# Kernel tuning notes

Hardware: AMD Instinct MI355X
Metric: run time of the kernel (lower is better)

The kernel has to match this reference:

```python
import jax, jax.numpy as jnp
import numpy as np

V = 32000
MASK_ID = 31999
EPS = 1e-3          # log-linear schedule eps
DT = 0.05           # reverse-step size
NUCLEUS_P = 0.9
NEG_INF = -1000000.0
B, S = 2, 1024


def move_chance(t):
    # BD3-LM log-linear schedule: move_chance(t) = (1 - eps) * t
    return (1.0 - EPS) * t


def nucleus_filter(probs, p):
    # descending sort over vocab
    order = jnp.argsort(-probs, axis=-1)                     # [B,S,V]
    sorted_probs = jnp.take_along_axis(probs, order, axis=-1)
    cum = jnp.cumsum(sorted_probs, axis=-1)
    keep = cum <= p
    keep = keep.at[..., 0].set(True)                          # always keep top-1
    kept = sorted_probs * keep
    inv = jnp.argsort(order, axis=-1)                         # inverse permutation
    filtered = jnp.take_along_axis(kept, inv, axis=-1)        # scatter back
    return filtered / jnp.sum(filtered, axis=-1, keepdims=True)


def setup_inputs() -> dict:
    key = jax.random.key(0)
    k1, k2, k3, k4 = jax.random.split(key, 4)
    x = jax.random.randint(k1, (B, S), 0, V, dtype=jnp.int32)
    m = jax.random.uniform(k4, (B, S)) < 0.5
    x = jnp.where(m, MASK_ID, x)
    logits = jax.random.normal(k2, (B, S, V), dtype=jnp.float32)
    t = jnp.ones((1,), dtype=jnp.float32)
    u = jax.random.uniform(k3, (B, S, V), dtype=jnp.float32)
    return {"x": x, "logits": logits, "t": t, "u": u}


def reference(x, logits, t, u):
    mct = move_chance(t)[..., None]          # [1,1]
    mcs = move_chance(t - DT)[..., None]     # [1,1]
    mask_prob = mcs / mct                    # [1,1], broadcasts over [S,V]

    logits = logits.at[:, :, MASK_ID].set(NEG_INF)
    p_x0 = jax.nn.softmax(logits, axis=-1)   # [B,S,V]
    p_x0 = nucleus_filter(p_x0, NUCLEUS_P)

    q_xs = p_x0 * (1.0 - mask_prob)
    q_xs = q_xs.at[:, :, MASK_ID].set(jnp.squeeze(mask_prob, -1))

    gumbel = -jnp.log(-jnp.log(u + 1e-10) + 1e-10)
    x_new = jnp.argmax(q_xs / (gumbel + 1e-10), axis=-1).astype(x.dtype)

    is_masked = x == MASK_ID
    x_new = jnp.where(is_masked, x_new, x)
    return x_new, p_x0
```

## Files before the change

kernel.cpp:

```cpp
#include <hip/hip_runtime.h>

#define NVOC 32000
#define NV4  (NVOC / 4)
#define MASKID 31999
#define NBINS2 2048
#define NTHR 512
#define NWAVES (NTHR / 64)
#define LISTCAP 2048

typedef unsigned int u32;
typedef unsigned long long u64;

__device__ __forceinline__ u32 fix32(float e) {
    float x = e * 4294967296.0f;
    x = fminf(x, 4294967040.0f);
    return (u32)x;
}

__device__ __forceinline__ int zbin(float t) {
    int b = (int)floorf(t);
    b = b < 0 ? 0 : b;
    return b > (NBINS2 - 1) ? (NBINS2 - 1) : b;
}
__device__ __forceinline__ float elq(float t, int b) {
    return __expf((t - (float)(b + 1)) * 0.015625f);
}

__global__ __launch_bounds__(NTHR, 8) void mdlm_kernel(
    const int* __restrict__ xin,
    const float* __restrict__ logits,
    const float* __restrict__ tin,
    const float* __restrict__ uin,
    float* __restrict__ out,
    int rows)
{
    __shared__ u64 sHist[NBINS2];
    __shared__ float sTab[NBINS2];
    __shared__ u32 sList[LISTCAP];
    __shared__ double sRedD[NWAVES];
    __shared__ int sRedI[NWAVES];
    __shared__ float sTT;
    __shared__ int sCnt, sB, sCross, sMaxDrop, sBref;
    __shared__ u32 sTau;
    __shared__ u64 sPart;
    __shared__ double sAsD, sSfpD, sScaleB;

    double* sD = (double*)sHist;

    const int row = blockIdx.x;
    if (row >= rows) return;
    const int tid = threadIdx.x;
    const float4* lrow4 = (const float4*)(logits + (size_t)row * NVOC);
    const float4* urow4 = (const float4*)(uin + (size_t)row * NVOC);
    float* prow = out + (size_t)rows + (size_t)row * NVOC;

#pragma unroll
    for (int k = 0; k < 4; ++k) sHist[tid + k * NTHR] = 0ULL;
    if (tid == 0) {
        sCnt = 0; sB = -1; sCross = 0; sMaxDrop = -1; sBref = -1;
        sTau = 0xFFFFFFFFu; sPart = 0ULL;
        sTT = tin[0];
    }
    __syncthreads();

    for (int v4 = tid; v4 < NV4; v4 += NTHR) {
        float4 f = lrow4[v4];
        if (v4 == (MASKID >> 2)) f.w = -1000000.0f;
        float zz[4] = {f.x, f.y, f.z, f.w};
#pragma unroll
        for (int e4 = 0; e4 < 4; ++e4) {
            float t = fmaf(zz[e4], 64.0f, 1024.0f);
            int b = zbin(t);
            u32 m = fix32(elq(t, b));
            atomicAdd(&sHist[b], (u64)m);
        }
    }
    __syncthreads();

#pragma unroll
    for (int k = 0; k < 4; ++k) {
        int s = tid + k * NTHR;
        if (sHist[s] != 0ULL) atomicMax(&sBref, s);
    }
    __syncthreads();
    const int bref = sBref;

#pragma unroll
    for (int k = 0; k < 4; ++k) {
        int s = tid + k * NTHR;
        double sc = exp((double)(s - bref) * 0.015625);
        sTab[s] = (float)sc;
        u64 H = sHist[s];
        sD[s] = (double)H * sc;
    }
    __syncthreads();

    for (int dlt = 1; dlt < NBINS2; dlt <<= 1) {
        double a0 = (tid + dlt < NBINS2) ? sD[tid + dlt] : 0.0;
        double a1 = (tid + NTHR + dlt < NBINS2) ? sD[tid + NTHR + dlt] : 0.0;
        double a2 = (tid + 2 * NTHR + dlt < NBINS2) ? sD[tid + 2 * NTHR + dlt] : 0.0;
        double a3 = (tid + 3 * NTHR + dlt < NBINS2) ? sD[tid + 3 * NTHR + dlt] : 0.0;
        __syncthreads();
        sD[tid] += a0;
        sD[tid + NTHR] += a1;
        sD[tid + 2 * NTHR] += a2;
        sD[tid + 3 * NTHR] += a3;
        __syncthreads();
    }
    const double T = 0.9 * sD[0];

#pragma unroll
    for (int k = 0; k < 4; ++k) {
        int s = tid + k * NTHR;
        double Ai = sD[s];
        double As = (s + 1 < NBINS2) ? sD[s + 1] : 0.0;
        bool dropped = (As >= T);
        bool keptf = (Ai <= T);
        if (dropped) atomicMax(&sMaxDrop, s);
        if (!dropped && !keptf) { sB = s; sCross = 1; }
    }
    __syncthreads();
    if (tid == 0) {
        int B = sCross ? sB : sMaxDrop;
        sB = B;
        double As = (B + 1 < NBINS2) ? sD[B + 1] : 0.0;
        if (B < 0) As = sD[0];
        sAsD = As;
        sSfpD = As;
        sScaleB = (B >= 0) ? exp((double)(B - bref) * 0.015625) : 1.0;
    }
    __syncthreads();

    const int Bst = sB;
    const int cross = sCross;
    const double AsD = sAsD;
    const double dScaleB = sScaleB;

    if (cross) {
        for (int v4 = tid; v4 < NV4; v4 += NTHR) {
            float4 f = lrow4[v4];
            if (v4 == (MASKID >> 2)) f.w = -1000000.0f;
            float zz[4] = {f.x, f.y, f.z, f.w};
#pragma unroll
            for (int e4 = 0; e4 < 4; ++e4) {
                float t = fmaf(zz[e4], 64.0f, 1024.0f);
                int b = zbin(t);
                if (b == Bst) {
                    u32 m = fix32(elq(t, b));
                    int pos = atomicAdd(&sCnt, 1);
                    if (pos < LISTCAP) sList[pos] = m;
                }
            }
        }
        __syncthreads();
        const int K = sCnt < LISTCAP ? sCnt : LISTCAP;
        for (int jj = tid; jj < K; jj += NTHR) {
            u32 mj = sList[jj];
            u64 isum = 0ULL;
            for (int q2 = 0; q2 < K; ++q2) {
                u32 mv = sList[q2];
                if (mv >= mj) isum += (u64)mv;
            }
            double s = AsD + (double)isum * dScaleB;
            if (s <= T) atomicMin(&sTau, mj);
        }
        __syncthreads();
        u32 tl = sTau;
        if (tl != 0xFFFFFFFFu) {
            u64 part = 0ULL;
            for (int q2 = tid; q2 < K; q2 += NTHR) {
                u32 mv = sList[q2];
                if (mv >= tl) part += (u64)mv;
            }
            if (part) atomicAdd(&sPart, part);
        }
        __syncthreads();
        if (tid == 0 && tl != 0xFFFFFFFFu)
            sSfpD = AsD + (double)sPart * dScaleB;
        __syncthreads();
    }

    const u32 tauU = (cross && sTau != 0xFFFFFFFFu) ? sTau : 0xFFFFFFFFu;
    const double SfpD = sSfpD;
    const float invSf = (float)(4294967296.0 / SfpD);

#pragma unroll
    for (int k = 0; k < 4; ++k) {
        int s = tid + k * NTHR;
        sTab[s] *= invSf;
    }

    double mpd, omd;
    {
        double td = (double)sTT;
        mpd = ((1.0 - 1e-3) * (td - 0.05)) / ((1.0 - 1e-3) * td);
        omd = 1.0 - mpd;
    }
    const float mqf = (float)(mpd / omd);
    __syncthreads();

    float r1 = -3.0e38f, r2 = -3.0e38f;
    float q1 = 0.0f,     q2 = 0.0f;
    int   i1 = 0,        i2 = 0;
    for (int v4 = tid; v4 < NV4; v4 += NTHR) {
        float4 uf = urow4[v4];
        float4 f = lrow4[v4];
        if (v4 == (MASKID >> 2)) f.w = -1000000.0f;
        float zz[4] = {f.x, f.y, f.z, f.w};
        float uu[4] = {uf.x, uf.y, uf.z, uf.w};
        float pp[4];
        const int i0 = v4 * 4;
#pragma unroll
        for (int e4 = 0; e4 < 4; ++e4) {
            float t = fmaf(zz[e4], 64.0f, 1024.0f);
            int b = zbin(t);
            float el = elq(t, b);
            bool kept = (b > Bst) || (b == Bst && fix32(el) >= tauU);
            float p = kept ? el * sTab[b] : 0.0f;
            pp[e4] = p;
            float g = -__logf(1e-10f - __logf(uu[e4] + 1e-10f));
            float r = p * __builtin_amdgcn_rcpf(g + 1e-10f);
            if (r > r1)      { r2 = r1; q2 = q1; i2 = i1; r1 = r; q1 = p; i1 = i0 + e4; }
            else if (r > r2) { r2 = r;  q2 = p;  i2 = i0 + e4; }
        }
        float4 po;
        po.x = pp[0]; po.y = pp[1]; po.z = pp[2]; po.w = pp[3];
        ((float4*)prow)[v4] = po;
    }
    if (tid == ((MASKID >> 2) % NTHR)) {
        float um = ((const float*)urow4)[MASKID];
        float g = -__logf(1e-10f - __logf(um + 1e-10f));
        float rm = mqf * __builtin_amdgcn_rcpf(g + 1e-10f);
        if (rm > r1)      { r2 = r1; q2 = q1; i2 = i1; r1 = rm; q1 = 0.0f; i1 = MASKID; }
        else if (rm > r2) { r2 = rm; q2 = 0.0f; i2 = MASKID; }
    }

    double best; int bidx;
    {
        const float* urowf = (const float*)urow4;
        double qa = (i1 == MASKID) ? mpd : (double)q1 * omd;
        double g1 = -log(-log((double)urowf[i1] + 1e-10) + 1e-10);
        best = qa / (g1 + 1e-10);
        bidx = i1;
        double qb = (i2 == MASKID) ? mpd : (double)q2 * omd;
        double g2 = -log(-log((double)urowf[i2] + 1e-10) + 1e-10);
        double rd = qb / (g2 + 1e-10);
        if (rd > best || (rd == best && i2 < bidx)) { best = rd; bidx = i2; }
    }

    for (int off = 32; off > 0; off >>= 1) {
        double ov = __shfl_down(best, off, 64);
        int oi = __shfl_down(bidx, off, 64);
        if (ov > best || (ov == best && oi < bidx)) { best = ov; bidx = oi; }
    }
    if ((tid & 63) == 0) { sRedD[tid >> 6] = best; sRedI[tid >> 6] = bidx; }
    __syncthreads();
    if (tid == 0) {
        best = sRedD[0]; bidx = sRedI[0];
        for (int w = 1; w < NWAVES; ++w) {
            double ov = sRedD[w]; int oi = sRedI[w];
            if (ov > best || (ov == best && oi < bidx)) { best = ov; bidx = oi; }
        }
        int xv = xin[row];
        out[row] = (float)((xv == MASKID) ? bidx : xv);
    }
}

extern "C" void kernel_launch(void* const* d_in, const int* in_sizes, int n_in,
                              void* d_out, int out_size, void* d_ws, size_t ws_size,
                              hipStream_t stream) {
    const int* x = (const int*)d_in[0];
    const float* logits = (const float*)d_in[1];
    const float* t = (const float*)d_in[2];
    const float* u = (const float*)d_in[3];
    float* out = (float*)d_out;
    const int rows = in_sizes[0];
    hipLaunchKernelGGL(mdlm_kernel, dim3(rows), dim3(NTHR), 0, stream,
                       x, logits, t, u, out, rows);
}
```

Measured before the change: 257.8 us.

## Prune Gumbel argmax to candidates with u near 1/e, with exact fallback

The main vocab loop no longer computes the double-log Gumbel noise and a running top-2 for every element. It records the max kept probability and collects indices whose u lies in a narrow band around 1/e, where the Gumbel denominator is close to zero and the ratio is largest. The argmax is then evaluated exactly, in double precision, over that candidate list plus the mask token. If the winner does not clear a bound of qmax*(1-mask_prob)*100, or the list overflows, a full second pass re-reads u and the written probabilities to compute the exact argmax. This removes transcendental work from the hot loop, at the cost of shared-memory atomics, extra barriers and an occasional second full pass.

```diff
diff --git a/kernel.cpp b/kernel.cpp
--- a/kernel.cpp
+++ b/kernel.cpp
@@ -7,6 +7,10 @@
 #define NTHR 512
 #define NWAVES (NTHR / 64)
 #define LISTCAP 2048
+
+#define ULO_F 0.36419f
+#define UHI_F 0.37157f
+#define INV_G0 100.0
 
 typedef unsigned int u32;
 typedef unsigned long long u64;
@@ -39,8 +43,9 @@
     __shared__ u32 sList[LISTCAP];
     __shared__ double sRedD[NWAVES];
     __shared__ int sRedI[NWAVES];
-    __shared__ float sTT;
-    __shared__ int sCnt, sB, sCross, sMaxDrop, sBref;
+    __shared__ float sRedF[NWAVES];
+    __shared__ float sTT, sQmaxF;
+    __shared__ int sCnt, sCntB, sB, sCross, sMaxDrop, sBref, sNeed;
     __shared__ u32 sTau;
     __shared__ u64 sPart;
     __shared__ double sAsD, sSfpD, sScaleB;
@@ -52,13 +57,14 @@
     const int tid = threadIdx.x;
     const float4* lrow4 = (const float4*)(logits + (size_t)row * NVOC);
     const float4* urow4 = (const float4*)(uin + (size_t)row * NVOC);
+    const float* urowf = (const float*)urow4;
     float* prow = out + (size_t)rows + (size_t)row * NVOC;
 
 #pragma unroll
     for (int k = 0; k < 4; ++k) sHist[tid + k * NTHR] = 0ULL;
     if (tid == 0) {
-        sCnt = 0; sB = -1; sCross = 0; sMaxDrop = -1; sBref = -1;
-        sTau = 0xFFFFFFFFu; sPart = 0ULL;
+        sCnt = 0; sCntB = 0; sB = -1; sCross = 0; sMaxDrop = -1; sBref = -1;
+        sTau = 0xFFFFFFFFu; sPart = 0ULL; sNeed = 0;
         sTT = tin[0];
     }
     __syncthreads();
@@ -181,14 +187,10 @@
     }
 
     const u32 tauU = (cross && sTau != 0xFFFFFFFFu) ? sTau : 0xFFFFFFFFu;
-    const double SfpD = sSfpD;
-    const float invSf = (float)(4294967296.0 / SfpD);
-
-#pragma unroll
-    for (int k = 0; k < 4; ++k) {
-        int s = tid + k * NTHR;
-        sTab[s] *= invSf;
-    }
+    const float invSf = (float)(4294967296.0 / sSfpD);
+
+#pragma unroll
+    for (int k = 0; k < 4; ++k) sTab[tid + k * NTHR] *= invSf;
 
     double mpd, omd;
     {
@@ -196,12 +198,9 @@
         mpd = ((1.0 - 1e-3) * (td - 0.05)) / ((1.0 - 1e-3) * td);
         omd = 1.0 - mpd;
     }
-    const float mqf = (float)(mpd / omd);
-    __syncthreads();
-
-    float r1 = -3.0e38f, r2 = -3.0e38f;
-    float q1 = 0.0f,     q2 = 0.0f;
-    int   i1 = 0,        i2 = 0;
+    __syncthreads();
+
+    float maxp = 0.0f;
     for (int v4 = tid; v4 < NV4; v4 += NTHR) {
         float4 uf = urow4[v4];
         float4 f = lrow4[v4];
@@ -218,36 +217,47 @@
             bool kept = (b > Bst) || (b == Bst && fix32(el) >= tauU);
             float p = kept ? el * sTab[b] : 0.0f;
             pp[e4] = p;
-            float g = -__logf(1e-10f - __logf(uu[e4] + 1e-10f));
-            float r = p * __builtin_amdgcn_rcpf(g + 1e-10f);
-            if (r > r1)      { r2 = r1; q2 = q1; i2 = i1; r1 = r; q1 = p; i1 = i0 + e4; }
-            else if (r > r2) { r2 = r;  q2 = p;  i2 = i0 + e4; }
+            maxp = fmaxf(maxp, p);
+            if (uu[e4] >= ULO_F && uu[e4] <= UHI_F) {
+                int pos = atomicAdd(&sCntB, 1);
+                if (pos < LISTCAP) sList[pos] = (u32)(i0 + e4);
+            }
         }
         float4 po;
         po.x = pp[0]; po.y = pp[1]; po.z = pp[2]; po.w = pp[3];
         ((float4*)prow)[v4] = po;
     }
-    if (tid == ((MASKID >> 2) % NTHR)) {
-        float um = ((const float*)urow4)[MASKID];
-        float g = -__logf(1e-10f - __logf(um + 1e-10f));
-        float rm = mqf * __builtin_amdgcn_rcpf(g + 1e-10f);
-        if (rm > r1)      { r2 = r1; q2 = q1; i2 = i1; r1 = rm; q1 = 0.0f; i1 = MASKID; }
-        else if (rm > r2) { r2 = rm; q2 = 0.0f; i2 = MASKID; }
-    }
-
-    double best; int bidx;
+    __syncthreads();
+
+    for (int off = 32; off > 0; off >>= 1)
+        maxp = fmaxf(maxp, __shfl_down(maxp, off, 64));
+    if ((tid & 63) == 0) sRedF[tid >> 6] = maxp;
+    __syncthreads();
+    if (tid == 0) {
+        float m = sRedF[0];
+        for (int w = 1; w < NWAVES; ++w) m = fmaxf(m, sRedF[w]);
+        sQmaxF = m;
+    }
+
+    double best = -1.0e300; int bidx = NVOC;
     {
-        const float* urowf = (const float*)urow4;
-        double qa = (i1 == MASKID) ? mpd : (double)q1 * omd;
-        double g1 = -log(-log((double)urowf[i1] + 1e-10) + 1e-10);
-        best = qa / (g1 + 1e-10);
-        bidx = i1;
-        double qb = (i2 == MASKID) ? mpd : (double)q2 * omd;
-        double g2 = -log(-log((double)urowf[i2] + 1e-10) + 1e-10);
-        double rd = qb / (g2 + 1e-10);
-        if (rd > best || (rd == best && i2 < bidx)) { best = rd; bidx = i2; }
-    }
-
+        const int K = sCntB < LISTCAP ? sCntB : LISTCAP;
+        for (int jj = tid; jj < K; jj += NTHR) {
+            int i = (int)sList[jj];
+            float up = urowf[i];
+            float pf = prow[i];
+            double q = (double)pf * omd;
+            double g = -log(-log((double)up + 1e-10) + 1e-10);
+            double r = q / (g + 1e-10);
+            if (r > best || (r == best && i < bidx)) { best = r; bidx = i; }
+        }
+        if (tid == 0) {
+            float um = urowf[MASKID];
+            double gm = -log(-log((double)um + 1e-10) + 1e-10);
+            double rm = mpd / (gm + 1e-10);
+            if (rm > best || (rm == best && MASKID < bidx)) { best = rm; bidx = MASKID; }
+        }
+    }
     for (int off = 32; off > 0; off >>= 1) {
         double ov = __shfl_down(best, off, 64);
         int oi = __shfl_down(bidx, off, 64);
@@ -261,8 +271,49 @@
             double ov = sRedD[w]; int oi = sRedI[w];
             if (ov > best || (ov == best && oi < bidx)) { best = ov; bidx = oi; }
         }
-        int xv = xin[row];
-        out[row] = (float)((xv == MASKID) ? bidx : xv);
+        double bound = (double)sQmaxF * omd * INV_G0;
+        int need = (sCntB > LISTCAP) || !(best > bound);
+        sNeed = need;
+        if (!need) {
+            int xv = xin[row];
+            out[row] = (float)((xv == MASKID) ? bidx : xv);
+        }
+    }
+    __syncthreads();
+
+    if (sNeed) {
+        double fb = -1.0e300; int fi = NVOC;
+        for (int v4 = tid; v4 < NV4; v4 += NTHR) {
+            float4 uf = urow4[v4];
+            float4 pf4 = ((const float4*)prow)[v4];
+            float uu[4] = {uf.x, uf.y, uf.z, uf.w};
+            float pp[4] = {pf4.x, pf4.y, pf4.z, pf4.w};
+            const int i0 = v4 * 4;
+#pragma unroll
+            for (int e4 = 0; e4 < 4; ++e4) {
+                const int i = i0 + e4;
+                double q = (i == MASKID) ? mpd : (double)pp[e4] * omd;
+                double g = -log(-log((double)uu[e4] + 1e-10) + 1e-10);
+                double r = q / (g + 1e-10);
+                if (r > fb || (r == fb && i < fi)) { fb = r; fi = i; }
+            }
+        }
+        for (int off = 32; off > 0; off >>= 1) {
+            double ov = __shfl_down(fb, off, 64);
+            int oi = __shfl_down(fi, off, 64);
+            if (ov > fb || (ov == fb && oi < fi)) { fb = ov; fi = oi; }
+        }
+        if ((tid & 63) == 0) { sRedD[tid >> 6] = fb; sRedI[tid >> 6] = fi; }
+        __syncthreads();
+        if (tid == 0) {
+            fb = sRedD[0]; fi = sRedI[0];
+            for (int w = 1; w < NWAVES; ++w) {
+                double ov = sRedD[w]; int oi = sRedI[w];
+                if (ov > fb || (ov == fb && oi < fi)) { fb = ov; fi = oi; }
+            }
+            int xv = xin[row];
+            out[row] = (float)((xv == MASKID) ? fi : xv);
+        }
     }
 }
 
```

Result: slower. 326.9 us (+26.8%).
